# Kernel optimization log

Hardware: AMD Instinct MI355X
Metric: run time of the kernel (lower is better)

The kernel has to match this reference:

```python
import jax, jax.numpy as jnp
import numpy as np

N, E, D, H, O = 50000, 800000, 128, 128, 64


def setup_inputs() -> dict:
    key = jax.random.key(0)
    ks = jax.random.split(key, 16)
    x = jax.random.normal(ks[0], (N, D), jnp.float32)
    edge_index = jax.random.randint(ks[1], (2, E), 0, N, dtype=jnp.int32).astype(jnp.int64)

    def lin_w(k, out_d, in_d):
        return jax.random.normal(k, (out_d, in_d), jnp.float32) * (1.0 / np.sqrt(in_d))

    return {
        "x": x,
        "edge_index": edge_index,
        # SAGEConv layer 0 (D -> H): lin_l acts on aggregated neighbors (with bias), lin_r on root (no bias)
        "Wl0": lin_w(ks[2], H, D), "bl0": jnp.zeros((H,), jnp.float32), "Wr0": lin_w(ks[3], H, D),
        # SAGEConv layers 1,2 (H -> H)
        "Wl1": lin_w(ks[4], H, H), "bl1": jnp.zeros((H,), jnp.float32), "Wr1": lin_w(ks[5], H, H),
        "Wl2": lin_w(ks[6], H, H), "bl2": jnp.zeros((H,), jnp.float32), "Wr2": lin_w(ks[7], H, H),
        # post_mp: Linear(H,H) -> Dropout -> Linear(H,O)
        "Wp1": lin_w(ks[8], H, H), "bp1": jnp.zeros((H,), jnp.float32),
        "Wp2": lin_w(ks[9], O, H), "bp2": jnp.zeros((O,), jnp.float32),
    }


def _sage_conv(x, src, dst, W_l, b_l, W_r, n_nodes):
    # mean-aggregate neighbor features: scatter messages x[src] onto dst
    msgs = x[src]                                              # [E, F] gather
    agg = jax.ops.segment_sum(msgs, dst, num_segments=n_nodes)  # [N, F]
    cnt = jax.ops.segment_sum(jnp.ones((src.shape[0],), x.dtype), dst, num_segments=n_nodes)
    mean = agg / jnp.maximum(cnt, 1.0)[:, None]
    return mean @ W_l.T + b_l + x @ W_r.T


def reference(x, edge_index, Wl0, bl0, Wr0, Wl1, bl1, Wr1, Wl2, bl2, Wr2, Wp1, bp1, Wp2, bp2):
    src, dst = edge_index[0], edge_index[1]
    n_nodes = x.shape[0]
    layers = [(Wl0, bl0, Wr0), (Wl1, bl1, Wr1), (Wl2, bl2, Wr2)]
    h = x
    for (W_l, b_l, W_r) in layers:
        h = _sage_conv(h, src, dst, W_l, b_l, W_r, n_nodes)
        h = jax.nn.relu(h)
        # dropout is identity at inference (training=False)
    h = h @ Wp1.T + bp1
    h = h @ Wp2.T + bp2
    return jax.nn.log_softmax(h, axis=1)
```

## Files before the change

kernel.cpp:

```cpp
#include <hip/hip_runtime.h>

using s16x8 = __attribute__((ext_vector_type(8))) short;
using f32x4 = __attribute__((ext_vector_type(4))) float;

#define NBUKMAX 512
#define BCAP    3072
#define CHUNK   4096

static __device__ __forceinline__ float bf2f(unsigned short u){
  union { unsigned int i; float f; } v; v.i = ((unsigned)u) << 16; return v.f;
}
static __device__ __forceinline__ unsigned short f2bf(float f){
  union { float f; unsigned int i; } v; v.f = f;
  unsigned int x = v.i;
  return (unsigned short)((x + 0x7fffu + ((x >> 16) & 1u)) >> 16);
}

__global__ void k_binit(const int* __restrict__ ei, int nc, int* __restrict__ flag,
                        int* __restrict__ gcur){
  int b = blockIdx.x*256 + threadIdx.x;
  if (b < NBUKMAX) gcur[b] = b * BCAP;
  if (blockIdx.x == 0 && threadIdx.x == 0){
    int all0 = 1;
    for (int i = 1; i < 2*nc; i += 2) if (ei[i] != 0) { all0 = 0; break; }
    flag[0] = all0;
  }
}

__global__ __launch_bounds__(256) void k_bscatter(const int* __restrict__ ei, int E,
                                                  int* __restrict__ gcur,
                                                  unsigned int* __restrict__ tmp,
                                                  const int* __restrict__ flag){
  __shared__ unsigned int pk[CHUNK];
  __shared__ unsigned short bk[CHUNK];
  __shared__ int hist[NBUKMAX];
  __shared__ int cur[NBUKMAX];
  int tid = threadIdx.x;
  for (int j = tid; j < NBUKMAX; j += 256) hist[j] = 0;
  __syncthreads();
  int is64 = flag[0];
  int base = blockIdx.x * CHUNK;
  int m = E - base; if (m > CHUNK) m = CHUNK;
  for (int j = tid; j < m; j += 256){
    int i = base + j;
    int s = is64 ? ei[2*(size_t)i] : ei[i];
    int d = is64 ? ei[2*((size_t)E + i)] : ei[(size_t)E + i];
    pk[j] = ((unsigned)(d & 127) << 25) | (unsigned)s;
    int b = d >> 7;
    bk[j] = (unsigned short)b;
    atomicAdd(&hist[b], 1);
  }
  __syncthreads();
  for (int b = tid; b < NBUKMAX; b += 256){
    int r = hist[b];
    cur[b] = (r > 0) ? atomicAdd(&gcur[b], r) : 0;
  }
  __syncthreads();
  for (int j = tid; j < m; j += 256){
    int b = bk[j];
    int p = atomicAdd(&cur[b], 1);
    if (p < (b + 1) * BCAP) tmp[p] = pk[j];
  }
}

__global__ void k_bscan(const int* __restrict__ gcur, int* __restrict__ bbase, int nbk){
  int lane = threadIdx.x & 63;
  int carry = 0;
  for (int b0 = 0; b0 < NBUKMAX; b0 += 64){
    int b = b0 + lane;
    int sz = 0;
    if (b < nbk){ sz = gcur[b] - b * BCAP; if (sz > BCAP) sz = BCAP; if (sz < 0) sz = 0; }
    int s = sz;
    #pragma unroll
    for (int off = 1; off < 64; off <<= 1){
      int u = __shfl_up(s, off, 64);
      if (lane >= off) s += u;
    }
    bbase[b] = carry + s - sz;
    carry += __shfl(s, 63, 64);
  }
}

__global__ __launch_bounds__(256) void k_binfill(const unsigned int* __restrict__ tmp,
                                                 const int* __restrict__ gcur,
                                                 const int* __restrict__ bbase,
                                                 int* __restrict__ rowp,
                                                 int* __restrict__ srcs, int N){
  __shared__ int hist[128], cur[128];
  __shared__ unsigned int stg[BCAP];
  __shared__ int lout[BCAP];
  int b = blockIdx.x;
  int d0 = b << 7;
  int nd = N - d0; if (nd > 128) nd = 128;
  int n = gcur[b] - b * BCAP; if (n > BCAP) n = BCAP; if (n < 0) n = 0;
  int obase = bbase[b];
  int tid = threadIdx.x;
  for (int j = tid; j < 128; j += 256) hist[j] = 0;
  __syncthreads();
  const unsigned int* reg = tmp + (size_t)b * BCAP;
  for (int i = tid; i < n; i += 256){
    unsigned int w = reg[i];
    stg[i] = w;
    atomicAdd(&hist[w >> 25], 1);
  }
  __syncthreads();
  if (tid < 64){
    int a  = hist[2*tid];
    int b2 = hist[2*tid+1];
    int ps = a + b2;
    int s = ps;
    #pragma unroll
    for (int off = 1; off < 64; off <<= 1){
      int u = __shfl_up(s, off, 64);
      if (tid >= off) s += u;
    }
    int ep = s - ps;
    cur[2*tid]   = ep;
    cur[2*tid+1] = ep + a;
    if (2*tid   < nd) rowp[d0 + 2*tid]   = obase + ep;
    if (2*tid+1 < nd) rowp[d0 + 2*tid+1] = obase + ep + a;
  }
  if (b == (int)gridDim.x - 1 && tid == 0) rowp[N] = obase + n;
  __syncthreads();
  for (int i = tid; i < n; i += 256){
    unsigned int w = stg[i];
    int p = atomicAdd(&cur[w >> 25], 1);
    lout[p] = (int)(w & 0x1FFFFFFu);
  }
  __syncthreads();
  for (int i = tid; i < n; i += 256) srcs[obase + i] = lout[i];
}

__global__ __launch_bounds__(256) void k_cvt4(const float* __restrict__ in,
                                              unsigned short* __restrict__ out, int n4){
  int i = blockIdx.x*blockDim.x + threadIdx.x;
  if (i >= n4) return;
  float4 v = ((const float4*)in)[i];
  ushort4 o; o.x = f2bf(v.x); o.y = f2bf(v.y); o.z = f2bf(v.z); o.w = f2bf(v.w);
  ((ushort4*)out)[i] = o;
}

__global__ __launch_bounds__(256) void k_prep(const float* __restrict__ w0, const float* __restrict__ w1,
                                              const float* __restrict__ w2, const float* __restrict__ w3,
                                              const float* __restrict__ w4, const float* __restrict__ w5,
                                              unsigned short* __restrict__ o0, unsigned short* __restrict__ o1,
                                              unsigned short* __restrict__ o2, unsigned short* __restrict__ o3,
                                              unsigned short* __restrict__ o4, unsigned short* __restrict__ o5,
                                              const float* __restrict__ Wp1, const float* __restrict__ bp1,
                                              const float* __restrict__ Wp2, const float* __restrict__ bp2,
                                              unsigned short* __restrict__ Wc, float* __restrict__ bc){
  int job = blockIdx.y;
  if (job < 6){
    if (blockIdx.x >= 16) return;
    const float* in; unsigned short* out;
    switch (job){
      case 0: in = w0; out = o0; break;
      case 1: in = w1; out = o1; break;
      case 2: in = w2; out = o2; break;
      case 3: in = w3; out = o3; break;
      case 4: in = w4; out = o4; break;
      default: in = w5; out = o5; break;
    }
    int i = blockIdx.x*256 + threadIdx.x;
    float4 v = ((const float4*)in)[i];
    ushort4 o; o.x = f2bf(v.x); o.y = f2bf(v.y); o.z = f2bf(v.z); o.w = f2bf(v.w);
    ((ushort4*)out)[i] = o;
  } else {
    int idx = blockIdx.x*256 + threadIdx.x;
    if (idx >= 64*128) return;
    int o = idx >> 7, k = idx & 127;
    float s = 0.f;
    for (int j = 0; j < 128; ++j) s += Wp2[o*128 + j] * Wp1[j*128 + k];
    Wc[o*128 + k] = f2bf(s);
    if (k == 0){
      float t = bp2[o];
      for (int j = 0; j < 128; ++j) t += Wp2[o*128 + j] * bp1[j];
      bc[o] = t;
    }
  }
}

__global__ __launch_bounds__(256) void k_agg(const unsigned short* __restrict__ h,
                                             const int* __restrict__ rowp,
                                             const int* __restrict__ srcs,
                                             unsigned short* __restrict__ mean, int N){
  int node = blockIdx.x*4 + (threadIdx.x >> 6);
  if (node >= N) return;
  int lane = threadIdx.x & 63;
  int g  = lane >> 4;
  int fl = lane & 15;
  int beg = rowp[node], end = rowp[node+1];
  int deg = end - beg;
  if (deg <= 0){
    if (g == 0){
      uint4 z = make_uint4(0,0,0,0);
      *(uint4*)(mean + (size_t)node*128 + fl*8) = z;
    }
    return;
  }
  float acc[8];
  #pragma unroll
  for (int f = 0; f < 8; ++f) acc[f] = 0.f;
  int last = end - 1;
  for (int base = beg; base < end; base += 16){
    int si[4]; float w[4]; uint4 v[4];
    #pragma unroll
    for (int s = 0; s < 4; ++s){
      int sl = base + s*4 + g;
      w[s] = (sl < end) ? 1.f : 0.f;
      si[s] = srcs[sl < end ? sl : last];
    }
    #pragma unroll
    for (int s = 0; s < 4; ++s) v[s] = *(const uint4*)(h + (size_t)si[s]*128 + fl*8);
    #pragma unroll
    for (int s = 0; s < 4; ++s){
      #pragma unroll
      for (int q = 0; q < 4; ++q){
        unsigned int wd = ((const unsigned int*)&v[s])[q];
        acc[2*q]   = fmaf(w[s], bf2f((unsigned short)(wd & 0xffffu)), acc[2*q]);
        acc[2*q+1] = fmaf(w[s], bf2f((unsigned short)(wd >> 16)),     acc[2*q+1]);
      }
    }
  }
  #pragma unroll
  for (int f = 0; f < 8; ++f){
    acc[f] += __shfl_xor(acc[f], 16, 64);
    acc[f] += __shfl_xor(acc[f], 32, 64);
  }
  if (g == 0){
    float inv = 1.f / (float)deg;
    unsigned int o[4];
    #pragma unroll
    for (int q = 0; q < 4; ++q)
      o[q] = ((unsigned int)f2bf(acc[2*q+1]*inv) << 16) | f2bf(acc[2*q]*inv);
    *(uint4*)(mean + (size_t)node*128 + fl*8) = *(uint4*)&o[0];
  }
}

__global__ __launch_bounds__(256) void k_gemm(const unsigned short* __restrict__ mean,
                                              const unsigned short* __restrict__ hin,
                                              const unsigned short* __restrict__ Wl,
                                              const unsigned short* __restrict__ Wr,
                                              const float* __restrict__ bias,
                                              unsigned short* __restrict__ hout, int N){
  __shared__ unsigned short wlds[64*512];
  int wave = threadIdx.x >> 6;
  int lane = threadIdx.x & 63;
  int lr = lane & 15;
  int kg = lane >> 4;

  #pragma unroll
  for (int cc = 0; cc < 16; ++cc){
    int c = wave + cc*4;
    const unsigned short* W = (c < 32) ? Wl : Wr;
    int jt = (c >> 2) & 7, t = c & 3;
    s16x8 v = *(const s16x8*)(W + (size_t)(jt*16 + lr)*128 + t*32 + kg*8);
    *(s16x8*)(wlds + (size_t)c*512 + lane*8) = v;
  }
  __syncthreads();

  int row0 = (blockIdx.x*4 + wave) * 16;
  if (row0 >= N) return;
  int row = row0 + lr; if (row >= N) row = N - 1;

  s16x8 a[8];
  const unsigned short* mrow = mean + (size_t)row*128;
  const unsigned short* hrow = hin  + (size_t)row*128;
  #pragma unroll
  for (int t = 0; t < 4; ++t) a[t]   = *(const s16x8*)(mrow + t*32 + kg*8);
  #pragma unroll
  for (int t = 0; t < 4; ++t) a[4+t] = *(const s16x8*)(hrow + t*32 + kg*8);

  #pragma unroll
  for (int jt = 0; jt < 8; ++jt){
    f32x4 acc = {0.f, 0.f, 0.f, 0.f};
    #pragma unroll
    for (int t = 0; t < 4; ++t){
      s16x8 b = *(const s16x8*)(wlds + (size_t)(jt*4 + t)*512 + lane*8);
      acc = __builtin_amdgcn_mfma_f32_16x16x32_bf16(a[t], b, acc, 0, 0, 0);
    }
    #pragma unroll
    for (int t = 0; t < 4; ++t){
      s16x8 b = *(const s16x8*)(wlds + (size_t)(32 + jt*4 + t)*512 + lane*8);
      acc = __builtin_amdgcn_mfma_f32_16x16x32_bf16(a[4+t], b, acc, 0, 0, 0);
    }
    int ocol = jt*16 + lr;
    float bv = bias[ocol];
    #pragma unroll
    for (int i = 0; i < 4; ++i){
      int orow = row0 + kg*4 + i;
      if (orow < N){
        float v = acc[i] + bv;
        v = fmaxf(v, 0.f);
        hout[(size_t)orow*128 + ocol] = f2bf(v);
      }
    }
  }
}

__global__ __launch_bounds__(256) void k_post(const unsigned short* __restrict__ h,
                                              const unsigned short* __restrict__ Wc,
                                              const float* __restrict__ bc,
                                              float* __restrict__ out, int N){
  int wave = threadIdx.x >> 6;
  int lane = threadIdx.x & 63;
  int row0 = (blockIdx.x*4 + wave) * 16;
  if (row0 >= N) return;
  int lr = lane & 15;
  int kg = lane >> 4;
  int row = row0 + lr; if (row >= N) row = N - 1;

  s16x8 a[4];
  const unsigned short* hrow = h + (size_t)row*128;
  #pragma unroll
  for (int t = 0; t < 4; ++t) a[t] = *(const s16x8*)(hrow + t*32 + kg*8);

  float v[4][4];
  #pragma unroll
  for (int jt = 0; jt < 4; ++jt){
    f32x4 acc = {0.f, 0.f, 0.f, 0.f};
    int j = jt*16 + lr;
    const unsigned short* wrow = Wc + (size_t)j*128;
    #pragma unroll
    for (int t = 0; t < 4; ++t){
      s16x8 b = *(const s16x8*)(wrow + t*32 + kg*8);
      acc = __builtin_amdgcn_mfma_f32_16x16x32_bf16(a[t], b, acc, 0, 0, 0);
    }
    float bv = bc[jt*16 + lr];
    #pragma unroll
    for (int i = 0; i < 4; ++i) v[jt][i] = acc[i] + bv;
  }

  #pragma unroll
  for (int i = 0; i < 4; ++i){
    float m = v[0][i];
    #pragma unroll
    for (int jt = 1; jt < 4; ++jt) m = fmaxf(m, v[jt][i]);
    #pragma unroll
    for (int msk = 1; msk < 16; msk <<= 1) m = fmaxf(m, __shfl_xor(m, msk, 64));
    float s = 0.f;
    #pragma unroll
    for (int jt = 0; jt < 4; ++jt) s += expf(v[jt][i] - m);
    #pragma unroll
    for (int msk = 1; msk < 16; msk <<= 1) s += __shfl_xor(s, msk, 64);
    float lse = m + logf(s);
    int orow = row0 + kg*4 + i;
    if (orow < N){
      #pragma unroll
      for (int jt = 0; jt < 4; ++jt)
        out[(size_t)orow*64 + jt*16 + lr] = v[jt][i] - lse;
    }
  }
}

extern "C" void kernel_launch(void* const* d_in, const int* in_sizes, int n_in,
                              void* d_out, int out_size, void* d_ws, size_t ws_size,
                              hipStream_t stream){
  const int N = in_sizes[0] / 128;
  const int E = in_sizes[1] / 2;
  if (N <= 0 || E <= 0) return;

  const float* x   = (const float*)d_in[0];
  const int*   ei  = (const int*)d_in[1];
  const float* Wl[3] = {(const float*)d_in[2], (const float*)d_in[5], (const float*)d_in[8]};
  const float* bl[3] = {(const float*)d_in[3], (const float*)d_in[6], (const float*)d_in[9]};
  const float* Wr[3] = {(const float*)d_in[4], (const float*)d_in[7], (const float*)d_in[10]};
  const float* Wp1 = (const float*)d_in[11];
  const float* bp1 = (const float*)d_in[12];
  const float* Wp2 = (const float*)d_in[13];
  const float* bp2 = (const float*)d_in[14];
  float* out = (float*)d_out;

  char* p = (char*)d_ws;
  auto alloc = [&](size_t bytes){ char* r = p; p += (bytes + 255) & ~(size_t)255; return r; };
  unsigned short* xb   = (unsigned short*)alloc((size_t)N*128*2);
  unsigned short* hA   = (unsigned short*)alloc((size_t)N*128*2);
  unsigned short* hB   = (unsigned short*)alloc((size_t)N*128*2);
  unsigned short* mean = (unsigned short*)alloc((size_t)N*128*2);
  unsigned short* wlb[3], *wrb[3];
  for (int l = 0; l < 3; ++l){
    wlb[l] = (unsigned short*)alloc(128*128*2);
    wrb[l] = (unsigned short*)alloc(128*128*2);
  }
  unsigned short* wc = (unsigned short*)alloc(64*128*2);
  float* bc   = (float*)alloc(64*4);
  int* rowp   = (int*)alloc((size_t)(N+1)*4);
  int* srcs   = (int*)alloc((size_t)E*4);
  int* eflag  = (int*)alloc(4);
  int* gcur   = (int*)alloc((size_t)NBUKMAX*4);
  int* bbase  = (int*)alloc((size_t)NBUKMAX*4);
  unsigned int* tmp = (unsigned int*)alloc((size_t)NBUKMAX*BCAP*4);

  int nbk = (N + 127) >> 7;

  k_binit<<<2, 256, 0, stream>>>(ei, (E < 64 ? E : 64), eflag, gcur);
  k_bscatter<<<(E + CHUNK - 1)/CHUNK, 256, 0, stream>>>(ei, E, gcur, tmp, eflag);
  k_bscan<<<1, 64, 0, stream>>>(gcur, bbase, nbk);
  k_binfill<<<nbk, 256, 0, stream>>>(tmp, gcur, bbase, rowp, srcs, N);

  k_cvt4<<<((N*128/4) + 255)/256, 256, 0, stream>>>(x, xb, N*128/4);
  k_prep<<<dim3(32, 7), 256, 0, stream>>>(Wl[0], Wr[0], Wl[1], Wr[1], Wl[2], Wr[2],
                                          wlb[0], wrb[0], wlb[1], wrb[1], wlb[2], wrb[2],
                                          Wp1, bp1, Wp2, bp2, wc, bc);

  int waves = (N + 15)/16;
  int gblocks = (waves + 3)/4;
  const unsigned short* hin = xb;
  unsigned short* houts[3] = {hA, hB, hA};
  for (int l = 0; l < 3; ++l){
    k_agg<<<(N + 3)/4, 256, 0, stream>>>(hin, rowp, srcs, mean, N);
    k_gemm<<<gblocks, 256, 0, stream>>>(mean, hin, wlb[l], wrb[l], bl[l], houts[l], N);
    hin = houts[l];
  }
  k_post<<<gblocks, 256, 0, stream>>>(hin, wc, bc, out, N);
}
```

Before: 212.8 us.

## Split mean aggregation into feature slices across blocks for cache locality

The aggregation kernel now divides the 128 features into four 32-feature slices, each handled by a separate range of blocks. Within a wave, four nodes are processed at once, with 4 edge groups and 4 lanes per 16-lane group. The intent is a smaller working set of gathered rows per pass, so L2/MALL hit rates improve for random neighbor gathers. The cost is that edge indices are read four times, and each gather is a 64-byte piece of a row instead of the full row.

```diff
diff --git a/kernel.cpp b/kernel.cpp
--- a/kernel.cpp
+++ b/kernel.cpp
@@ -183,21 +183,23 @@
 __global__ __launch_bounds__(256) void k_agg(const unsigned short* __restrict__ h,
                                              const int* __restrict__ rowp,
                                              const int* __restrict__ srcs,
-                                             unsigned short* __restrict__ mean, int N){
-  int node = blockIdx.x*4 + (threadIdx.x >> 6);
-  if (node >= N) return;
+                                             unsigned short* __restrict__ mean,
+                                             int N, int nbs){
+  int bid = blockIdx.x;
+  int slice = bid / nbs;
+  int bis = bid - slice * nbs;
+  int wid = threadIdx.x >> 6;
   int lane = threadIdx.x & 63;
-  int g  = lane >> 4;
-  int fl = lane & 15;
-  int beg = rowp[node], end = rowp[node+1];
+  int ng  = lane >> 4;
+  int sub = lane & 15;
+  int es  = sub >> 2;
+  int q   = sub & 3;
+  int node = (bis*4 + wid)*4 + ng;
+  bool valid = node < N;
+  int beg = 0, end = 0;
+  if (valid){ beg = rowp[node]; end = rowp[node+1]; }
   int deg = end - beg;
-  if (deg <= 0){
-    if (g == 0){
-      uint4 z = make_uint4(0,0,0,0);
-      *(uint4*)(mean + (size_t)node*128 + fl*8) = z;
-    }
-    return;
-  }
+  const unsigned short* hs = h + slice*32 + q*8;
   float acc[8];
   #pragma unroll
   for (int f = 0; f < 8; ++f) acc[f] = 0.f;
@@ -206,34 +208,34 @@
     int si[4]; float w[4]; uint4 v[4];
     #pragma unroll
     for (int s = 0; s < 4; ++s){
-      int sl = base + s*4 + g;
+      int sl = base + s*4 + es;
       w[s] = (sl < end) ? 1.f : 0.f;
       si[s] = srcs[sl < end ? sl : last];
     }
     #pragma unroll
-    for (int s = 0; s < 4; ++s) v[s] = *(const uint4*)(h + (size_t)si[s]*128 + fl*8);
+    for (int s = 0; s < 4; ++s) v[s] = *(const uint4*)(hs + (size_t)si[s]*128);
     #pragma unroll
     for (int s = 0; s < 4; ++s){
       #pragma unroll
-      for (int q = 0; q < 4; ++q){
-        unsigned int wd = ((const unsigned int*)&v[s])[q];
-        acc[2*q]   = fmaf(w[s], bf2f((unsigned short)(wd & 0xffffu)), acc[2*q]);
-        acc[2*q+1] = fmaf(w[s], bf2f((unsigned short)(wd >> 16)),     acc[2*q+1]);
+      for (int c = 0; c < 4; ++c){
+        unsigned int wd = ((const unsigned int*)&v[s])[c];
+        acc[2*c]   = fmaf(w[s], bf2f((unsigned short)(wd & 0xffffu)), acc[2*c]);
+        acc[2*c+1] = fmaf(w[s], bf2f((unsigned short)(wd >> 16)),     acc[2*c+1]);
       }
     }
   }
   #pragma unroll
   for (int f = 0; f < 8; ++f){
-    acc[f] += __shfl_xor(acc[f], 16, 64);
-    acc[f] += __shfl_xor(acc[f], 32, 64);
-  }
-  if (g == 0){
-    float inv = 1.f / (float)deg;
+    acc[f] += __shfl_xor(acc[f], 4, 64);
+    acc[f] += __shfl_xor(acc[f], 8, 64);
+  }
+  if (valid && es == 0){
+    float inv = 1.f / fmaxf((float)deg, 1.f);
     unsigned int o[4];
     #pragma unroll
-    for (int q = 0; q < 4; ++q)
-      o[q] = ((unsigned int)f2bf(acc[2*q+1]*inv) << 16) | f2bf(acc[2*q]*inv);
-    *(uint4*)(mean + (size_t)node*128 + fl*8) = *(uint4*)&o[0];
+    for (int c = 0; c < 4; ++c)
+      o[c] = ((unsigned int)f2bf(acc[2*c+1]*inv) << 16) | f2bf(acc[2*c]*inv);
+    *(uint4*)(mean + (size_t)node*128 + slice*32 + q*8) = *(uint4*)&o[0];
   }
 }
 
@@ -405,10 +407,11 @@
 
   int waves = (N + 15)/16;
   int gblocks = (waves + 3)/4;
+  int nbs = (N + 15)/16;
   const unsigned short* hin = xb;
   unsigned short* houts[3] = {hA, hB, hA};
   for (int l = 0; l < 3; ++l){
-    k_agg<<<(N + 3)/4, 256, 0, stream>>>(hin, rowp, srcs, mean, N);
+    k_agg<<<4*nbs, 256, 0, stream>>>(hin, rowp, srcs, mean, N, nbs);
     k_gemm<<<gblocks, 256, 0, stream>>>(mean, hin, wlb[l], wrb[l], bl[l], houts[l], N);
     hin = houts[l];
   }
```

New measurement: 238.5 us. 12.1% more time.

## Fuse neighbor aggregation into SAGE GEMM and fold bucket scan into binfill

Applied to the files above, without the earlier changes.

Merges the mean-aggregation kernel and the dense GEMM kernel into a single kernel per layer. Each block aggregates 64 nodes into LDS, then runs MFMA against weights staged in two K-halves to keep shared memory small. This removes the global mean buffer round trip and one launch per layer. It also drops the separate bucket-scan kernel: each binfill block recomputes its own prefix offset from gcur. The trade-offs are redundant scan work across blocks and lower parallelism in aggregation (one wave handles 16 nodes serially), so gather latency is harder to hide.

```diff
diff --git a/kernel.cpp b/kernel.cpp
--- a/kernel.cpp
+++ b/kernel.cpp
@@ -63,40 +63,39 @@
   }
 }
 
-__global__ void k_bscan(const int* __restrict__ gcur, int* __restrict__ bbase, int nbk){
-  int lane = threadIdx.x & 63;
-  int carry = 0;
-  for (int b0 = 0; b0 < NBUKMAX; b0 += 64){
-    int b = b0 + lane;
-    int sz = 0;
-    if (b < nbk){ sz = gcur[b] - b * BCAP; if (sz > BCAP) sz = BCAP; if (sz < 0) sz = 0; }
-    int s = sz;
-    #pragma unroll
-    for (int off = 1; off < 64; off <<= 1){
-      int u = __shfl_up(s, off, 64);
-      if (lane >= off) s += u;
-    }
-    bbase[b] = carry + s - sz;
-    carry += __shfl(s, 63, 64);
-  }
-}
-
 __global__ __launch_bounds__(256) void k_binfill(const unsigned int* __restrict__ tmp,
                                                  const int* __restrict__ gcur,
-                                                 const int* __restrict__ bbase,
                                                  int* __restrict__ rowp,
-                                                 int* __restrict__ srcs, int N){
+                                                 int* __restrict__ srcs, int N, int nbk){
   __shared__ int hist[128], cur[128];
   __shared__ unsigned int stg[BCAP];
   __shared__ int lout[BCAP];
+  __shared__ int sh_obase;
   int b = blockIdx.x;
   int d0 = b << 7;
   int nd = N - d0; if (nd > 128) nd = 128;
   int n = gcur[b] - b * BCAP; if (n > BCAP) n = BCAP; if (n < 0) n = 0;
-  int obase = bbase[b];
   int tid = threadIdx.x;
   for (int j = tid; j < 128; j += 256) hist[j] = 0;
-  __syncthreads();
+  if (tid < 64){
+    int lane = tid;
+    int carry = 0;
+    for (int b0 = 0; b0 <= b; b0 += 64){
+      int bb = b0 + lane;
+      int sz = 0;
+      if (bb < nbk){ int t2 = gcur[bb] - bb*BCAP; sz = t2 < 0 ? 0 : (t2 > BCAP ? BCAP : t2); }
+      int s = sz;
+      #pragma unroll
+      for (int off = 1; off < 64; off <<= 1){
+        int u = __shfl_up(s, off, 64);
+        if (lane >= off) s += u;
+      }
+      if (bb == b) sh_obase = carry + s - sz;
+      carry += __shfl(s, 63, 64);
+    }
+  }
+  __syncthreads();
+  int obase = sh_obase;
   const unsigned int* reg = tmp + (size_t)b * BCAP;
   for (int i = tid; i < n; i += 256){
     unsigned int w = reg[i];
@@ -120,7 +119,7 @@
     if (2*tid   < nd) rowp[d0 + 2*tid]   = obase + ep;
     if (2*tid+1 < nd) rowp[d0 + 2*tid+1] = obase + ep + a;
   }
-  if (b == (int)gridDim.x - 1 && tid == 0) rowp[N] = obase + n;
+  if (b == nbk - 1 && tid == 0) rowp[N] = obase + n;
   __syncthreads();
   for (int i = tid; i < n; i += 256){
     unsigned int w = stg[i];
@@ -180,119 +179,144 @@
   }
 }
 
-__global__ __launch_bounds__(256) void k_agg(const unsigned short* __restrict__ h,
-                                             const int* __restrict__ rowp,
-                                             const int* __restrict__ srcs,
-                                             unsigned short* __restrict__ mean, int N){
-  int node = blockIdx.x*4 + (threadIdx.x >> 6);
-  if (node >= N) return;
-  int lane = threadIdx.x & 63;
-  int g  = lane >> 4;
-  int fl = lane & 15;
-  int beg = rowp[node], end = rowp[node+1];
-  int deg = end - beg;
-  if (deg <= 0){
-    if (g == 0){
-      uint4 z = make_uint4(0,0,0,0);
-      *(uint4*)(mean + (size_t)node*128 + fl*8) = z;
-    }
-    return;
-  }
-  float acc[8];
-  #pragma unroll
-  for (int f = 0; f < 8; ++f) acc[f] = 0.f;
-  int last = end - 1;
-  for (int base = beg; base < end; base += 16){
-    int si[4]; float w[4]; uint4 v[4];
-    #pragma unroll
-    for (int s = 0; s < 4; ++s){
-      int sl = base + s*4 + g;
-      w[s] = (sl < end) ? 1.f : 0.f;
-      si[s] = srcs[sl < end ? sl : last];
-    }
-    #pragma unroll
-    for (int s = 0; s < 4; ++s) v[s] = *(const uint4*)(h + (size_t)si[s]*128 + fl*8);
-    #pragma unroll
-    for (int s = 0; s < 4; ++s){
-      #pragma unroll
-      for (int q = 0; q < 4; ++q){
-        unsigned int wd = ((const unsigned int*)&v[s])[q];
-        acc[2*q]   = fmaf(w[s], bf2f((unsigned short)(wd & 0xffffu)), acc[2*q]);
-        acc[2*q+1] = fmaf(w[s], bf2f((unsigned short)(wd >> 16)),     acc[2*q+1]);
-      }
-    }
-  }
-  #pragma unroll
-  for (int f = 0; f < 8; ++f){
-    acc[f] += __shfl_xor(acc[f], 16, 64);
-    acc[f] += __shfl_xor(acc[f], 32, 64);
-  }
-  if (g == 0){
-    float inv = 1.f / (float)deg;
-    unsigned int o[4];
-    #pragma unroll
-    for (int q = 0; q < 4; ++q)
-      o[q] = ((unsigned int)f2bf(acc[2*q+1]*inv) << 16) | f2bf(acc[2*q]*inv);
-    *(uint4*)(mean + (size_t)node*128 + fl*8) = *(uint4*)&o[0];
-  }
-}
-
-__global__ __launch_bounds__(256) void k_gemm(const unsigned short* __restrict__ mean,
-                                              const unsigned short* __restrict__ hin,
-                                              const unsigned short* __restrict__ Wl,
-                                              const unsigned short* __restrict__ Wr,
-                                              const float* __restrict__ bias,
-                                              unsigned short* __restrict__ hout, int N){
-  __shared__ unsigned short wlds[64*512];
-  int wave = threadIdx.x >> 6;
-  int lane = threadIdx.x & 63;
+__global__ __launch_bounds__(256) void k_aggemm(const unsigned short* __restrict__ hin,
+                                                const int* __restrict__ rowp,
+                                                const int* __restrict__ srcs,
+                                                const unsigned short* __restrict__ Wl,
+                                                const unsigned short* __restrict__ Wr,
+                                                const float* __restrict__ bias,
+                                                unsigned short* __restrict__ hout, int N){
+  __shared__ unsigned short wlds[32*512];
+  __shared__ unsigned short mlds[64*130];
+  int tid  = threadIdx.x;
+  int wave = tid >> 6;
+  int lane = tid & 63;
   int lr = lane & 15;
   int kg = lane >> 4;
-
-  #pragma unroll
-  for (int cc = 0; cc < 16; ++cc){
+  int nb0 = blockIdx.x * 64;
+
+  #pragma unroll
+  for (int cc = 0; cc < 8; ++cc){
     int c = wave + cc*4;
-    const unsigned short* W = (c < 32) ? Wl : Wr;
-    int jt = (c >> 2) & 7, t = c & 3;
-    s16x8 v = *(const s16x8*)(W + (size_t)(jt*16 + lr)*128 + t*32 + kg*8);
+    const unsigned short* W = (c < 16) ? Wl : Wr;
+    int jt = (c >> 1) & 7, tt = c & 1;
+    s16x8 v = *(const s16x8*)(W + (size_t)(jt*16 + lr)*128 + tt*32 + kg*8);
     *(s16x8*)(wlds + (size_t)c*512 + lane*8) = v;
   }
-  __syncthreads();
-
-  int row0 = (blockIdx.x*4 + wave) * 16;
-  if (row0 >= N) return;
-  int row = row0 + lr; if (row >= N) row = N - 1;
-
-  s16x8 a[8];
-  const unsigned short* mrow = mean + (size_t)row*128;
-  const unsigned short* hrow = hin  + (size_t)row*128;
-  #pragma unroll
-  for (int t = 0; t < 4; ++t) a[t]   = *(const s16x8*)(mrow + t*32 + kg*8);
-  #pragma unroll
-  for (int t = 0; t < 4; ++t) a[4+t] = *(const s16x8*)(hrow + t*32 + kg*8);
-
-  #pragma unroll
-  for (int jt = 0; jt < 8; ++jt){
-    f32x4 acc = {0.f, 0.f, 0.f, 0.f};
-    #pragma unroll
-    for (int t = 0; t < 4; ++t){
-      s16x8 b = *(const s16x8*)(wlds + (size_t)(jt*4 + t)*512 + lane*8);
-      acc = __builtin_amdgcn_mfma_f32_16x16x32_bf16(a[t], b, acc, 0, 0, 0);
-    }
-    #pragma unroll
-    for (int t = 0; t < 4; ++t){
-      s16x8 b = *(const s16x8*)(wlds + (size_t)(32 + jt*4 + t)*512 + lane*8);
-      acc = __builtin_amdgcn_mfma_f32_16x16x32_bf16(a[4+t], b, acc, 0, 0, 0);
-    }
-    int ocol = jt*16 + lr;
-    float bv = bias[ocol];
-    #pragma unroll
-    for (int i = 0; i < 4; ++i){
-      int orow = row0 + kg*4 + i;
-      if (orow < N){
-        float v = acc[i] + bv;
-        v = fmaxf(v, 0.f);
-        hout[(size_t)orow*128 + ocol] = f2bf(v);
+
+  for (int r = 0; r < 16; ++r){
+    int node = nb0 + wave*16 + r;
+    int beg = 0, end = 0;
+    if (node < N){ beg = rowp[node]; end = rowp[node+1]; }
+    int deg = end - beg;
+    float acc[8];
+    #pragma unroll
+    for (int f = 0; f < 8; ++f) acc[f] = 0.f;
+    int last = end - 1;
+    for (int base = beg; base < end; base += 16){
+      int si[4]; float w[4]; uint4 v[4];
+      #pragma unroll
+      for (int s = 0; s < 4; ++s){
+        int sl = base + s*4 + kg;
+        w[s] = (sl < end) ? 1.f : 0.f;
+        si[s] = srcs[sl < end ? sl : last];
+      }
+      #pragma unroll
+      for (int s = 0; s < 4; ++s) v[s] = *(const uint4*)(hin + (size_t)si[s]*128 + lr*8);
+      #pragma unroll
+      for (int s = 0; s < 4; ++s){
+        #pragma unroll
+        for (int q = 0; q < 4; ++q){
+          unsigned int wd = ((const unsigned int*)&v[s])[q];
+          acc[2*q]   = fmaf(w[s], bf2f((unsigned short)(wd & 0xffffu)), acc[2*q]);
+          acc[2*q+1] = fmaf(w[s], bf2f((unsigned short)(wd >> 16)),     acc[2*q+1]);
+        }
+      }
+    }
+    #pragma unroll
+    for (int f = 0; f < 8; ++f){
+      acc[f] += __shfl_xor(acc[f], 16, 64);
+      acc[f] += __shfl_xor(acc[f], 32, 64);
+    }
+    if (kg == 0){
+      float inv = (deg > 0) ? 1.f/(float)deg : 0.f;
+      unsigned int o[4];
+      #pragma unroll
+      for (int q = 0; q < 4; ++q)
+        o[q] = ((unsigned int)f2bf(acc[2*q+1]*inv) << 16) | f2bf(acc[2*q]*inv);
+      *(uint4*)(mlds + (size_t)(wave*16 + r)*130 + lr*8) = *(uint4*)&o[0];
+    }
+  }
+  __syncthreads();
+
+  int row0 = nb0 + wave*16;
+  int rowc = row0 + lr; if (rowc >= N) rowc = N - 1;
+  const unsigned short* hrow = hin + (size_t)rowc*128;
+
+  f32x4 acc2[8];
+  #pragma unroll
+  for (int jt = 0; jt < 8; ++jt) acc2[jt] = (f32x4){0.f,0.f,0.f,0.f};
+
+  {
+    s16x8 am[2], ah[2];
+    #pragma unroll
+    for (int tt = 0; tt < 2; ++tt){
+      am[tt] = *(const s16x8*)(mlds + (size_t)(wave*16 + lr)*130 + tt*32 + kg*8);
+      ah[tt] = *(const s16x8*)(hrow + tt*32 + kg*8);
+    }
+    #pragma unroll
+    for (int jt = 0; jt < 8; ++jt){
+      #pragma unroll
+      for (int tt = 0; tt < 2; ++tt){
+        s16x8 bl_ = *(const s16x8*)(wlds + (size_t)(jt*2 + tt)*512 + lane*8);
+        acc2[jt] = __builtin_amdgcn_mfma_f32_16x16x32_bf16(am[tt], bl_, acc2[jt], 0, 0, 0);
+        s16x8 br_ = *(const s16x8*)(wlds + (size_t)(16 + jt*2 + tt)*512 + lane*8);
+        acc2[jt] = __builtin_amdgcn_mfma_f32_16x16x32_bf16(ah[tt], br_, acc2[jt], 0, 0, 0);
+      }
+    }
+  }
+  __syncthreads();
+  #pragma unroll
+  for (int cc = 0; cc < 8; ++cc){
+    int c = wave + cc*4;
+    const unsigned short* W = (c < 16) ? Wl : Wr;
+    int jt = (c >> 1) & 7, tt = c & 1;
+    s16x8 v = *(const s16x8*)(W + (size_t)(jt*16 + lr)*128 + (2 + tt)*32 + kg*8);
+    *(s16x8*)(wlds + (size_t)c*512 + lane*8) = v;
+  }
+  __syncthreads();
+  {
+    s16x8 am[2], ah[2];
+    #pragma unroll
+    for (int tt = 0; tt < 2; ++tt){
+      am[tt] = *(const s16x8*)(mlds + (size_t)(wave*16 + lr)*130 + (2 + tt)*32 + kg*8);
+      ah[tt] = *(const s16x8*)(hrow + (2 + tt)*32 + kg*8);
+    }
+    #pragma unroll
+    for (int jt = 0; jt < 8; ++jt){
+      #pragma unroll
+      for (int tt = 0; tt < 2; ++tt){
+        s16x8 bl_ = *(const s16x8*)(wlds + (size_t)(jt*2 + tt)*512 + lane*8);
+        acc2[jt] = __builtin_amdgcn_mfma_f32_16x16x32_bf16(am[tt], bl_, acc2[jt], 0, 0, 0);
+        s16x8 br_ = *(const s16x8*)(wlds + (size_t)(16 + jt*2 + tt)*512 + lane*8);
+        acc2[jt] = __builtin_amdgcn_mfma_f32_16x16x32_bf16(ah[tt], br_, acc2[jt], 0, 0, 0);
+      }
+    }
+  }
+
+  if (row0 < N){
+    #pragma unroll
+    for (int jt = 0; jt < 8; ++jt){
+      int ocol = jt*16 + lr;
+      float bv = bias[ocol];
+      #pragma unroll
+      for (int i = 0; i < 4; ++i){
+        int orow = row0 + kg*4 + i;
+        if (orow < N){
+          float v = acc2[jt][i] + bv;
+          v = fmaxf(v, 0.f);
+          hout[(size_t)orow*128 + ocol] = f2bf(v);
+        }
       }
     }
   }
@@ -376,7 +400,6 @@
   unsigned short* xb   = (unsigned short*)alloc((size_t)N*128*2);
   unsigned short* hA   = (unsigned short*)alloc((size_t)N*128*2);
   unsigned short* hB   = (unsigned short*)alloc((size_t)N*128*2);
-  unsigned short* mean = (unsigned short*)alloc((size_t)N*128*2);
   unsigned short* wlb[3], *wrb[3];
   for (int l = 0; l < 3; ++l){
     wlb[l] = (unsigned short*)alloc(128*128*2);
@@ -388,28 +411,24 @@
   int* srcs   = (int*)alloc((size_t)E*4);
   int* eflag  = (int*)alloc(4);
   int* gcur   = (int*)alloc((size_t)NBUKMAX*4);
-  int* bbase  = (int*)alloc((size_t)NBUKMAX*4);
   unsigned int* tmp = (unsigned int*)alloc((size_t)NBUKMAX*BCAP*4);
 
   int nbk = (N + 127) >> 7;
 
   k_binit<<<2, 256, 0, stream>>>(ei, (E < 64 ? E : 64), eflag, gcur);
   k_bscatter<<<(E + CHUNK - 1)/CHUNK, 256, 0, stream>>>(ei, E, gcur, tmp, eflag);
-  k_bscan<<<1, 64, 0, stream>>>(gcur, bbase, nbk);
-  k_binfill<<<nbk, 256, 0, stream>>>(tmp, gcur, bbase, rowp, srcs, N);
+  k_binfill<<<nbk, 256, 0, stream>>>(tmp, gcur, rowp, srcs, N, nbk);
 
   k_cvt4<<<((N*128/4) + 255)/256, 256, 0, stream>>>(x, xb, N*128/4);
   k_prep<<<dim3(32, 7), 256, 0, stream>>>(Wl[0], Wr[0], Wl[1], Wr[1], Wl[2], Wr[2],
                                           wlb[0], wrb[0], wlb[1], wrb[1], wlb[2], wrb[2],
                                           Wp1, bp1, Wp2, bp2, wc, bc);
 
-  int waves = (N + 15)/16;
-  int gblocks = (waves + 3)/4;
+  int gblocks = (N + 63)/64;
   const unsigned short* hin = xb;
   unsigned short* houts[3] = {hA, hB, hA};
   for (int l = 0; l < 3; ++l){
-    k_agg<<<(N + 3)/4, 256, 0, stream>>>(hin, rowp, srcs, mean, N);
-    k_gemm<<<gblocks, 256, 0, stream>>>(mean, hin, wlb[l], wrb[l], bl[l], houts[l], N);
+    k_aggemm<<<gblocks, 256, 0, stream>>>(hin, rowp, srcs, wlb[l], wrb[l], bl[l], houts[l], N);
     hin = houts[l];
   }
   k_post<<<gblocks, 256, 0, stream>>>(hin, wc, bc, out, N);
```

New measurement: 289.6 us. 1.36x slower.
